# Optimization experiments

Hardware: AMD Instinct MI355X
Metric: run time of the kernel (lower is better)

The kernel has to match this reference:

```python
import jax, jax.numpy as jnp
import numpy as np

THRESH = 0.7
MIN_KEPT = 100000
IGNORE_INDEX = -100


def setup_inputs() -> dict:
    key = jax.random.key(0)
    k1, k2 = jax.random.split(key)
    B, C, H, W = 8, 19, 512, 512
    logits = jax.random.normal(k1, (B, C, H, W), dtype=jnp.float32)
    targets = jax.random.randint(k2, (B, H, W), 0, C, dtype=jnp.int64)
    return {"logits": logits, "targets": targets}


def reference(logits, targets):
    B, C, H, W = logits.shape
    # softmax over class dim, then log(p + eps) as in the original
    probs = jax.nn.softmax(logits, axis=1)
    log_probs = jnp.log(probs + 1e-7)
    mask = (targets != IGNORE_INDEX)
    # per-pixel NLL: gather log-prob of the target class
    gathered = jnp.take_along_axis(log_probs, targets[:, None, :, :], axis=1)[:, 0]  # [B,H,W]
    losses = -gathered * mask.astype(logits.dtype)                                   # [B,H,W]
    losses_flat = losses.reshape(B, -1)                                              # [B,HW]
    n_pix = losses_flat.shape[1]
    # threshold index is static (Python ints), matching torch code exactly
    thresh_idx = max(MIN_KEPT, int(n_pix * THRESH))
    thresh_idx = min(thresh_idx, n_pix - 1)
    sorted_losses = jnp.sort(losses_flat, axis=1)
    thresh = sorted_losses[:, thresh_idx]                                            # [B]
    selected = losses_flat > thresh[:, None]                                         # [B,HW] bool
    # Faithful to the original (buggy-looking) loop:
    #   selected_mask[i, targets[i].flatten()] = 1
    # i.e. target *values* are used as indices into the flattened HW axis.
    tgt_flat = targets.reshape(B, -1)  # values in [0, C)
    selected = jax.vmap(lambda s, t: s.at[t].set(True))(selected, tgt_flat)
    return selected.reshape(B, H, W).astype(jnp.float32)
```

## Files before the change

kernel.cpp:

```cpp
#include <hip/hip_runtime.h>

#define NB 8
#define NC 19
#define HW (512*512)
#define NPIX (NB*HW)
#define RANK 183500u
#define NBIN 4096
#define CAP  4096

typedef float f32x2 __attribute__((ext_vector_type(2)));

__device__ __forceinline__ unsigned fkey(float f) {
    unsigned b = __float_as_uint(f);
    return (b & 0x80000000u) ? ~b : (b | 0x80000000u);
}
__device__ __forceinline__ float finv(unsigned u) {
    unsigned b = (u & 0x80000000u) ? (u & 0x7fffffffu) : ~u;
    return __uint_as_float(b);
}
__device__ __forceinline__ int bin_of(float l) {
    int b = (int)((l + 1.0f) * 224.0f);
    return b < 0 ? 0 : (b > NBIN - 1 ? NBIN - 1 : b);
}
__device__ __forceinline__ unsigned umn(unsigned a, unsigned b) { return a < b ? a : b; }
__device__ __forceinline__ unsigned umx(unsigned a, unsigned b) { return a > b ? a : b; }

__global__ __launch_bounds__(256) void losses_kernel(
    const float* __restrict__ logits, const int* __restrict__ targets,
    float* __restrict__ losses)
{
    const int blk  = blockIdx.x;
    const int tid  = threadIdx.x;
    const int pix0 = blk * 512;
    const int bb   = pix0 >> 18;
    const int pp   = pix0 & (HW - 1);
    const float* base = logits + (size_t)bb * NC * HW + pp;
    const unsigned voff = (unsigned)(tid * 8);

    f32x2 x[19];
    #pragma unroll
    for (int c = 0; c < NC; ++c)
        asm volatile("global_load_dwordx2 %0, %1, %2"
                     : "=v"(x[c]) : "v"(voff), "s"(base + (size_t)c * HW));

    int2 t2 = *reinterpret_cast<const int2*>(targets + pix0 + tid * 2);

    asm volatile("s_waitcnt vmcnt(0)" ::: "memory");
    __builtin_amdgcn_sched_barrier(0);

    const int tt[2] = {t2.x, t2.y};
    float oo[2];
    #pragma unroll
    for (int j = 0; j < 2; ++j) {
        const int t = tt[j];
        float m = x[0][j];
        #pragma unroll
        for (int c = 1; c < NC; ++c) m = fmaxf(m, x[c][j]);
        float s = 0.f, et = 0.f;
        #pragma unroll
        for (int c = 0; c < NC; ++c) {
            float e = expf(x[c][j] - m);
            s += e;
            if (c == t) et = e;
        }
        oo[j] = (t >= 0 && t < NC) ? -logf(et / s + 1e-7f) : 0.f;
    }
    *reinterpret_cast<float2*>(losses + pix0 + tid * 2) = make_float2(oo[0], oo[1]);
}

__global__ __launch_bounds__(256) void hist_kernel(
    const float* __restrict__ losses, const int* __restrict__ targets,
    unsigned* __restrict__ ghist, unsigned* __restrict__ present)
{
    __shared__ unsigned lh[NBIN];
    __shared__ unsigned pres;
    const int b = blockIdx.y;
    for (int j = threadIdx.x; j < NBIN; j += 256) lh[j] = 0;
    if (threadIdx.x == 0) pres = 0u;
    __syncthreads();
    const float4* L = reinterpret_cast<const float4*>(losses + (size_t)b * HW)
                      + (size_t)blockIdx.x * 1024;
    const int4* T = reinterpret_cast<const int4*>(targets + (size_t)b * HW)
                    + (size_t)blockIdx.x * 1024;
    unsigned bits = 0u;
    for (int j = threadIdx.x; j < 1024; j += 256) {
        float4 v = L[j];
        atomicAdd(&lh[bin_of(v.x)], 1u);
        atomicAdd(&lh[bin_of(v.y)], 1u);
        atomicAdd(&lh[bin_of(v.z)], 1u);
        atomicAdd(&lh[bin_of(v.w)], 1u);
        int4 tv = T[j];
        if (tv.x >= 0 && tv.x < NC) bits |= 1u << tv.x;
        if (tv.y >= 0 && tv.y < NC) bits |= 1u << tv.y;
        if (tv.z >= 0 && tv.z < NC) bits |= 1u << tv.z;
        if (tv.w >= 0 && tv.w < NC) bits |= 1u << tv.w;
    }
    #pragma unroll
    for (int o = 1; o < 64; o <<= 1) bits |= __shfl_xor(bits, o);
    if ((threadIdx.x & 63) == 0 && bits) atomicOr(&pres, bits);
    __syncthreads();
    unsigned* gh = ghist + b * NBIN;
    for (int j = threadIdx.x; j < NBIN; j += 256) {
        unsigned v = lh[j];
        if (v) atomicAdd(&gh[j], v);
    }
    if (threadIdx.x == 0 && pres) atomicOr(&present[b], pres);
}

__global__ __launch_bounds__(256) void compact_kernel(
    const float* __restrict__ losses, const unsigned* __restrict__ ghist,
    unsigned* __restrict__ count, float* __restrict__ cand,
    unsigned* __restrict__ info)
{
    __shared__ unsigned wsum[4], woff[4];
    __shared__ unsigned sh_T, sh_r;
    const int b = blockIdx.y;
    const int tid = threadIdx.x;
    const int lane = tid & 63, wid = tid >> 6;
    const unsigned* gh = ghist + b * NBIN;

    unsigned s = 0;
    #pragma unroll
    for (int j = 0; j < 16; ++j) s += gh[tid * 16 + j];
    unsigned incl = s;
    #pragma unroll
    for (int o = 1; o < 64; o <<= 1) {
        unsigned v = (unsigned)__shfl_up((int)incl, o);
        if (lane >= o) incl += v;
    }
    if (lane == 63) wsum[wid] = incl;
    __syncthreads();
    if (tid == 0) { unsigned c = 0; for (int w = 0; w < 4; ++w) { woff[w] = c; c += wsum[w]; } }
    __syncthreads();
    unsigned excl = woff[wid] + incl - s;
    if (RANK >= excl && RANK < excl + s) {
        unsigned rr = RANK - excl, cum = 0;
        for (int j = 0; j < 16; ++j) {
            unsigned c = gh[tid * 16 + j];
            if (cum + c > rr) {
                sh_T = (unsigned)(tid * 16 + j); sh_r = rr - cum;
                if (blockIdx.x == 0) { info[b * 2] = sh_T; info[b * 2 + 1] = sh_r; }
                break;
            }
            cum += c;
        }
    }
    __syncthreads();
    const int T = (int)sh_T;

    const float4* L = reinterpret_cast<const float4*>(losses + (size_t)b * HW)
                      + (size_t)blockIdx.x * 1024;
    for (int j = tid; j < 1024; j += 256) {
        float4 v = L[j];
        float vals[4] = {v.x, v.y, v.z, v.w};
        #pragma unroll
        for (int q = 0; q < 4; ++q) {
            float val = vals[q];
            bool sel = (bin_of(val) == T);
            unsigned long long msk = __ballot(sel);
            if (msk) {
                int leader = __ffsll(msk) - 1;
                int pre = __popcll(msk & ((1ull << lane) - 1ull));
                unsigned base = 0;
                if (lane == leader) base = atomicAdd(&count[b], (unsigned)__popcll(msk));
                base = (unsigned)__shfl((int)base, leader);
                if (sel) {
                    unsigned idx = base + (unsigned)pre;
                    if (idx < CAP) cand[b * CAP + idx] = val;
                }
            }
        }
    }
}

__global__ __launch_bounds__(256) void final_kernel(
    const float* __restrict__ cand, const unsigned* __restrict__ count,
    const unsigned* __restrict__ info, float* __restrict__ thresh)
{
    __shared__ unsigned kf[CAP];
    __shared__ unsigned h[512];
    __shared__ unsigned sub[2048];
    __shared__ unsigned red[8];
    __shared__ unsigned kmin_sh, shift_sh, sb_sh, r2_sh, cnt_sh;
    const int tid = threadIdx.x, b = blockIdx.x;
    unsigned k = count[b]; if (k > CAP) k = CAP;
    const unsigned r = info[b * 2 + 1];

    for (unsigned j = tid; j < k; j += 256) kf[j] = fkey(cand[b * CAP + j]);
    for (int j = tid; j < 512; j += 256) h[j] = 0;
    __syncthreads();

    unsigned lmin = 0xFFFFFFFFu, lmax = 0u;
    for (unsigned j = tid; j < k; j += 256) { unsigned v = kf[j]; lmin = umn(lmin, v); lmax = umx(lmax, v); }
    #pragma unroll
    for (int o = 1; o < 64; o <<= 1) {
        lmin = umn(lmin, (unsigned)__shfl_xor((int)lmin, o));
        lmax = umx(lmax, (unsigned)__shfl_xor((int)lmax, o));
    }
    if ((tid & 63) == 0) { red[tid >> 6] = lmin; red[4 + (tid >> 6)] = lmax; }
    __syncthreads();
    if (tid == 0) {
        unsigned mn = red[0], mx = red[4];
        for (int w = 1; w < 4; ++w) { mn = umn(mn, red[w]); mx = umx(mx, red[4 + w]); }
        unsigned spread = mx - mn;
        int bits = 32 - __clz((int)(spread | 1u));
        shift_sh = (unsigned)(bits > 9 ? bits - 9 : 0);
        kmin_sh = mn;
        cnt_sh = 0;
    }
    __syncthreads();
    const unsigned kmin = kmin_sh, shift = shift_sh;
    for (unsigned j = tid; j < k; j += 256) atomicAdd(&h[(kf[j] - kmin) >> shift], 1u);
    __syncthreads();
    if (tid == 0) {
        unsigned cum = 0; int sb = 0;
        while (sb < 511 && cum + h[sb] <= r) { cum += h[sb]; ++sb; }
        sb_sh = (unsigned)sb; r2_sh = r - cum;
    }
    __syncthreads();
    const unsigned sb = sb_sh;
    for (unsigned j = tid; j < k; j += 256) {
        if (((kf[j] - kmin) >> shift) == sb) {
            unsigned idx = atomicAdd(&cnt_sh, 1u);
            if (idx < 2048) sub[idx] = kf[j];
        }
    }
    __syncthreads();
    const unsigned k2 = umn(cnt_sh, 2048u), r2 = r2_sh;
    for (unsigned e = tid; e < k2; e += 256) {
        unsigned v = sub[e], less = 0, eq = 0;
        for (unsigned j = 0; j < k2; ++j) { unsigned u = sub[j]; less += (u < v); eq += (u == v); }
        if (less <= r2 && r2 < less + eq) thresh[b] = finv(v);
    }
}

__global__ __launch_bounds__(256) void emit_kernel(
    float* __restrict__ out, const float* __restrict__ thresh,
    const unsigned* __restrict__ present)
{
    int i4 = blockIdx.x * 256 + threadIdx.x;
    int i = i4 * 4;
    int b = i >> 18;
    int p = i & (HW - 1);
    float th = thresh[b];
    unsigned pm = present[b];
    float4 v = reinterpret_cast<float4*>(out)[i4];
    float4 o;
    o.x = ((v.x > th) || ((p + 0) < NC && ((pm >> (p + 0)) & 1u))) ? 1.f : 0.f;
    o.y = ((v.y > th) || ((p + 1) < NC && ((pm >> (p + 1)) & 1u))) ? 1.f : 0.f;
    o.z = ((v.z > th) || ((p + 2) < NC && ((pm >> (p + 2)) & 1u))) ? 1.f : 0.f;
    o.w = ((v.w > th) || ((p + 3) < NC && ((pm >> (p + 3)) & 1u))) ? 1.f : 0.f;
    reinterpret_cast<float4*>(out)[i4] = o;
}

extern "C" void kernel_launch(void* const* d_in, const int* in_sizes, int n_in,
                              void* d_out, int out_size, void* d_ws, size_t ws_size,
                              hipStream_t stream)
{
    const float* logits  = (const float*)d_in[0];
    const int*   targets = (const int*)d_in[1];
    float* out = (float*)d_out;

    char* ws = (char*)d_ws;
    unsigned* ghist   = (unsigned*)(ws);
    unsigned* count   = (unsigned*)(ws + 131072);
    unsigned* present = (unsigned*)(ws + 131104);
    unsigned* info    = (unsigned*)(ws + 131136);
    float*    thresh  = (float*)   (ws + 131200);
    float*    cand    = (float*)   (ws + 131232);

    hipMemsetAsync(d_ws, 0, 131232, stream);

    losses_kernel<<<NPIX / 512, 256, 0, stream>>>(logits, targets, out);
    hist_kernel<<<dim3(64, NB), 256, 0, stream>>>(out, targets, ghist, present);
    compact_kernel<<<dim3(64, NB), 256, 0, stream>>>(out, ghist, count, cand, info);
    final_kernel<<<NB, 256, 0, stream>>>(cand, count, info, thresh);
    emit_kernel<<<NPIX / 4 / 256, 256, 0, stream>>>(out, thresh, present);
}
```

Before: 109.4 us.

## Split loss pixels into staggered halves with pipelined waits and fuse workspace zeroing

Each thread now computes losses for two pixels from different halves of the image, offset by a stagger constant, using scalar dword loads. It waits only for the first pixel's loads before computing, so the second pixel's loads overlap with that math. The separate workspace memset is removed and the histogram/count region is zeroed inside the losses kernel instead. Coalescing per load instruction drops from dwordx2 to dword, and the zeroing relies on later kernels not reading unzeroed fields before writing them.

```diff
diff --git a/kernel.cpp b/kernel.cpp
--- a/kernel.cpp
+++ b/kernel.cpp
@@ -4,11 +4,11 @@
 #define NC 19
 #define HW (512*512)
 #define NPIX (NB*HW)
+#define HHW (HW/2)
 #define RANK 183500u
 #define NBIN 4096
 #define CAP  4096
-
-typedef float f32x2 __attribute__((ext_vector_type(2)));
+#define OFFB 69696
 
 __device__ __forceinline__ unsigned fkey(float f) {
     unsigned b = __float_as_uint(f);
@@ -27,45 +27,70 @@
 
 __global__ __launch_bounds__(256) void losses_kernel(
     const float* __restrict__ logits, const int* __restrict__ targets,
-    float* __restrict__ losses)
-{
-    const int blk  = blockIdx.x;
-    const int tid  = threadIdx.x;
-    const int pix0 = blk * 512;
-    const int bb   = pix0 >> 18;
-    const int pp   = pix0 & (HW - 1);
-    const float* base = logits + (size_t)bb * NC * HW + pp;
-    const unsigned voff = (unsigned)(tid * 8);
-
-    f32x2 x[19];
+    float* __restrict__ losses, unsigned* __restrict__ wszero)
+{
+    const int blk = blockIdx.x, tid = threadIdx.x;
+    if (blk < 33) {
+        int j = blk * 1024 + tid * 4;
+        if (j < 32784) *reinterpret_cast<uint4*>(wszero + j) = make_uint4(0u,0u,0u,0u);
+    }
+    const int b  = blk >> 9;
+    const int r  = ((blk & 511) << 8) + tid;
+    const int rB = (r + OFFB) & (HHW - 1);
+    const int pA = (b << 18) + r;
+    const int pB = (b << 18) + HHW + rB;
+    const float* cb = logits + (size_t)b * NC * HW;
+    const int*   tb = targets + (size_t)b * HW;
+    const unsigned vA = (unsigned)(r * 4);
+    const unsigned vB = (unsigned)((HHW + rB) * 4);
+
+    int tA, tB;
+    float xA[NC], xB[NC];
+    asm volatile("global_load_dword %0, %1, %2" : "=v"(tA) : "v"(vA), "s"(tb));
+    asm volatile("global_load_dword %0, %1, %2" : "=v"(tB) : "v"(vB), "s"(tb));
     #pragma unroll
     for (int c = 0; c < NC; ++c)
-        asm volatile("global_load_dwordx2 %0, %1, %2"
-                     : "=v"(x[c]) : "v"(voff), "s"(base + (size_t)c * HW));
-
-    int2 t2 = *reinterpret_cast<const int2*>(targets + pix0 + tid * 2);
-
-    asm volatile("s_waitcnt vmcnt(0)" ::: "memory");
+        asm volatile("global_load_dword %0, %1, %2"
+                     : "=v"(xA[c]) : "v"(vA), "s"(cb + (size_t)c * HW));
+    #pragma unroll
+    for (int c = 0; c < NC; ++c)
+        asm volatile("global_load_dword %0, %1, %2"
+                     : "=v"(xB[c]) : "v"(vB), "s"(cb + (size_t)c * HW));
+
+    asm volatile("s_waitcnt vmcnt(19)" ::: "memory");
     __builtin_amdgcn_sched_barrier(0);
 
-    const int tt[2] = {t2.x, t2.y};
-    float oo[2];
-    #pragma unroll
-    for (int j = 0; j < 2; ++j) {
-        const int t = tt[j];
-        float m = x[0][j];
-        #pragma unroll
-        for (int c = 1; c < NC; ++c) m = fmaxf(m, x[c][j]);
+    {
+        float m = xA[0];
+        #pragma unroll
+        for (int c = 1; c < NC; ++c) m = fmaxf(m, xA[c]);
         float s = 0.f, et = 0.f;
         #pragma unroll
         for (int c = 0; c < NC; ++c) {
-            float e = expf(x[c][j] - m);
+            float e = expf(xA[c] - m);
             s += e;
-            if (c == t) et = e;
-        }
-        oo[j] = (t >= 0 && t < NC) ? -logf(et / s + 1e-7f) : 0.f;
-    }
-    *reinterpret_cast<float2*>(losses + pix0 + tid * 2) = make_float2(oo[0], oo[1]);
+            if (c == tA) et = e;
+        }
+        losses[pA] = (tA >= 0 && tA < NC) ? -logf(et / s + 1e-7f) : 0.f;
+    }
+
+    __builtin_amdgcn_sched_barrier(0);
+    asm volatile("s_waitcnt vmcnt(1)" ::: "memory");
+    __builtin_amdgcn_sched_barrier(0);
+
+    {
+        float m = xB[0];
+        #pragma unroll
+        for (int c = 1; c < NC; ++c) m = fmaxf(m, xB[c]);
+        float s = 0.f, et = 0.f;
+        #pragma unroll
+        for (int c = 0; c < NC; ++c) {
+            float e = expf(xB[c] - m);
+            s += e;
+            if (c == tB) et = e;
+        }
+        losses[pB] = (tB >= 0 && tB < NC) ? -logf(et / s + 1e-7f) : 0.f;
+    }
 }
 
 __global__ __launch_bounds__(256) void hist_kernel(
@@ -269,9 +294,8 @@
     float*    thresh  = (float*)   (ws + 131200);
     float*    cand    = (float*)   (ws + 131232);
 
-    hipMemsetAsync(d_ws, 0, 131232, stream);
-
-    losses_kernel<<<NPIX / 512, 256, 0, stream>>>(logits, targets, out);
+
+    losses_kernel<<<NPIX / 512, 256, 0, stream>>>(logits, targets, out, ghist);
     hist_kernel<<<dim3(64, NB), 256, 0, stream>>>(out, targets, ghist, present);
     compact_kernel<<<dim3(64, NB), 256, 0, stream>>>(out, ghist, count, cand, info);
     final_kernel<<<NB, 256, 0, stream>>>(cand, count, info, thresh);
```

Result: faster. 106.1 us, median of 2 (-3.0%).
